# Performance work log

Hardware: AMD Instinct MI355X
Metric: run time of the kernel (lower is better)

## Reference

```python
import jax, jax.numpy as jnp
import numpy as np

D_MODEL = 1024
N_EXPERTS = 16
TOP_K = 2
NUM_TASKS = 8
D_TASK = 64
D_FFN = 32
LN_EPS = 1e-5


def setup_inputs() -> dict:
    key = jax.random.key(0)
    ks = jax.random.split(key, 8)
    B, S = 4, 4096
    s = 0.02
    return dict(
        x=jax.random.normal(ks[0], (B, S, D_MODEL), jnp.float32),
        task_id=jax.random.randint(ks[1], (B,), 0, NUM_TASKS),
        task_emb=jax.random.normal(ks[2], (NUM_TASKS, D_TASK), jnp.float32) * s,
        Wg=jax.random.normal(ks[3], (D_MODEL + D_TASK, N_EXPERTS), jnp.float32) * s,
        bg=jnp.zeros((N_EXPERTS,), jnp.float32),
        W1=jax.random.normal(ks[4], (N_EXPERTS, D_MODEL, D_FFN), jnp.float32) * s,
        b1=jnp.zeros((N_EXPERTS, D_FFN), jnp.float32),
        W2=jax.random.normal(ks[5], (N_EXPERTS, D_FFN, D_MODEL), jnp.float32) * s,
        b2=jnp.zeros((N_EXPERTS, D_MODEL), jnp.float32),
    )


def reference(x, task_id, task_emb, Wg, bg, W1, b1, W2, b2):
    B, S, D = x.shape
    # F.layer_norm(x, x.shape[1:]): normalize jointly over (seq, d_model), no affine
    mu = jnp.mean(x, axis=(1, 2), keepdims=True)
    var = jnp.var(x, axis=(1, 2), keepdims=True)
    x_norm = (x - mu) * jax.lax.rsqrt(var + LN_EPS)

    t_emb = jnp.broadcast_to(task_emb[task_id][:, None, :], (B, S, D_TASK))
    logits = jnp.concatenate([x_norm, t_emb], axis=-1) @ Wg + bg  # [B,S,E]

    topk_vals, topk_idx = jax.lax.top_k(logits, TOP_K)  # [B,S,K]
    topk_probs = jax.nn.softmax(topk_vals, axis=-1)

    # combine weights per token per expert: w[t,e] = sum_k prob * onehot(idx)
    oh = jax.nn.one_hot(topk_idx, N_EXPERTS, dtype=x.dtype)  # [B,S,K,E]
    w = jnp.einsum('bske,bsk->bse', oh, topk_probs).reshape(B * S, N_EXPERTS)

    xf = x.reshape(B * S, D)
    # all-expert FFN (d_ffn=32 -> small intermediate [T,E,32])
    h = jax.nn.silu(jnp.einsum('td,edf->tef', xf, W1) + b1)
    hw = h * w[:, :, None]  # apply combine weight before expanding back to d_model
    out = jnp.einsum('tef,efd->td', hw, W2) + w @ b2
    final = out.reshape(B, S, D)

    # load-balance loss from expert usage counts
    usage = jnp.sum(oh, axis=(0, 1, 2))  # [E]
    usage_mean = usage.mean() + 1e-6
    usage_std = jnp.std(usage, ddof=1)  # torch unbiased std
    lb_loss = (usage_std / usage_mean) ** 2
    return final, lb_loss, topk_idx
```

## Files before the change

kernel.cpp:

```cpp
#include <hip/hip_runtime.h>
#include <math.h>

#define D_MODEL 1024
#define N_EXP   16
#define SEQ     4096
#define NBATCH  4
#define NTOK    (NBATCH*SEQ)
#define DFFN    32
#define DTASK   64

#define WS_SUMS   0
#define WS_RS     64
#define WS_MU     80
#define WS_GB     128
#define WS_CNT    512
#define WS_TOKREC 1024
#define WS_BUCKET (1024 + NTOK*16)

#define OUT_LB  (NTOK*D_MODEL)
#define OUT_IDX (NTOK*D_MODEL + 1)

__device__ __forceinline__ void atomAddF(float* p, float v) {
  unsafeAtomicAdd(p, v);
}

__global__ __launch_bounds__(256) void k_stats(const float* __restrict__ x,
                                               double* __restrict__ sums) {
  int b = blockIdx.y;
  const float4* xb = (const float4*)(x + (size_t)b * SEQ * D_MODEL);
  const int n4 = SEQ * D_MODEL / 4;
  double s = 0.0, ss = 0.0;
  for (int i = blockIdx.x * 256 + threadIdx.x; i < n4; i += gridDim.x * 256) {
    float4 v = xb[i];
    s  += (double)v.x + (double)v.y + (double)v.z + (double)v.w;
    ss += (double)v.x*v.x + (double)v.y*v.y + (double)v.z*v.z + (double)v.w*v.w;
  }
  __shared__ double r0[256], r1[256];
  r0[threadIdx.x] = s; r1[threadIdx.x] = ss;
  __syncthreads();
  for (int off = 128; off > 0; off >>= 1) {
    if (threadIdx.x < off) { r0[threadIdx.x] += r0[threadIdx.x+off]; r1[threadIdx.x] += r1[threadIdx.x+off]; }
    __syncthreads();
  }
  if (threadIdx.x == 0) { atomicAdd(&sums[2*b], r0[0]); atomicAdd(&sums[2*b+1], r1[0]); }
}

__global__ __launch_bounds__(256) void k_prep(const double* __restrict__ sums,
    const int* __restrict__ task_id, const float* __restrict__ task_emb,
    const float* __restrict__ Wg, const float* __restrict__ bg,
    float* __restrict__ wsf) {
  __shared__ float smu[4], srs[4], sSe[16];
  __shared__ float red[16][16];
  int tid = threadIdx.x;
  if (tid < 4) {
    double n = (double)SEQ * (double)D_MODEL;
    double mu = sums[2*tid] / n;
    double var = sums[2*tid+1] / n - mu*mu;
    float rsv = (float)(1.0 / sqrt(var + 1e-5));
    smu[tid] = (float)mu; srs[tid] = rsv;
    wsf[WS_RS/4 + tid] = rsv; wsf[WS_MU/4 + tid] = (float)mu;
  }
  {
    int e = tid & 15, part = tid >> 4;
    float p = 0.f;
    for (int r = part*64; r < part*64 + 64; ++r) p += Wg[r*N_EXP + e];
    red[part][e] = p;
  }
  __syncthreads();
  if (tid < 16) {
    float t = 0.f;
    for (int i = 0; i < 16; ++i) t += red[i][tid];
    sSe[tid] = t;
  }
  __syncthreads();
  if (tid < 64) {
    int b = tid >> 4, e = tid & 15;
    int tk = task_id[b];
    float off = 0.f;
    for (int j = 0; j < DTASK; ++j)
      off += task_emb[tk*DTASK + j] * Wg[(D_MODEL + j)*N_EXP + e];
    wsf[WS_GB/4 + tid] = bg[e] + off - srs[b]*smu[b]*sSe[e];
  }
}

__global__ __launch_bounds__(256) void k_gating(const float* __restrict__ x,
    const float* __restrict__ Wg, const float* __restrict__ wsf,
    float* __restrict__ out, float4* __restrict__ tokrec,
    int* __restrict__ cnt, int* __restrict__ bucket) {
  __shared__ float wgT[N_EXP][D_MODEL + 1];
  __shared__ float lg[4][4][16];
  int tid = threadIdx.x;
  for (int i = tid; i < D_MODEL*N_EXP/4; i += 256) {
    float4 v = ((const float4*)Wg)[i];
    int d = i >> 2, e0 = (i & 3) << 2;
    wgT[e0+0][d] = v.x; wgT[e0+1][d] = v.y; wgT[e0+2][d] = v.z; wgT[e0+3][d] = v.w;
  }
  __syncthreads();
  int wave = tid >> 6, lane = tid & 63;
  int blk0 = blockIdx.x * 64;
  int b = blk0 >> 12;
  float rsb = wsf[WS_RS/4 + b];
  for (int it = 0; it < 4; ++it) {
    int tbase = blk0 + wave*16 + it*4;
    float xr[4][16];
    #pragma unroll
    for (int tt = 0; tt < 4; ++tt) {
      const float* xp = x + (size_t)(tbase + tt)*D_MODEL + lane;
      #pragma unroll
      for (int j = 0; j < 16; ++j) xr[tt][j] = xp[j*64];
    }
    float v[64];
    #pragma unroll
    for (int i = 0; i < 64; ++i) v[i] = 0.f;
    #pragma unroll
    for (int j = 0; j < 16; ++j) {
      int d = lane + 64*j;
      #pragma unroll
      for (int e = 0; e < 16; ++e) {
        float w = wgT[e][d];
        #pragma unroll
        for (int tt = 0; tt < 4; ++tt) v[tt*16 + e] = fmaf(xr[tt][j], w, v[tt*16 + e]);
      }
    }
    #pragma unroll
    for (int m = 32; m >= 1; m >>= 1) {
      #pragma unroll
      for (int j2 = 0; j2 < m; ++j2) {
        float lo = v[j2], hi = v[j2 + m];
        bool up = (lane & m) != 0;
        float mine = up ? hi : lo;
        float theirs = up ? lo : hi;
        v[j2] = mine + __shfl_xor(theirs, m, 64);
      }
    }
    int e = lane & 15, tt = lane >> 4;
    float logit = fmaf(rsb, v[0], wsf[WS_GB/4 + b*16 + e]);
    lg[wave][tt][e] = logit;
    __syncthreads();
    if ((lane & 15) == 0) {
      int token = tbase + tt;
      float v0 = -1e30f, v1 = -1e30f; int i0 = 0, i1 = 0;
      #pragma unroll
      for (int ee = 0; ee < 16; ++ee) {
        float L = lg[wave][tt][ee];
        if (L > v0)      { v1 = v0; i1 = i0; v0 = L; i0 = ee; }
        else if (L > v1) { v1 = L; i1 = ee; }
      }
      float ex = __expf(v1 - v0);
      float p0 = 1.f / (1.f + ex);
      float p1 = ex * p0;
      out[OUT_IDX + token*2 + 0] = (float)i0;
      out[OUT_IDX + token*2 + 1] = (float)i1;
      tokrec[token] = make_float4(__int_as_float(i0), __int_as_float(i1), p0, p1);
      int pos0 = atomicAdd(&cnt[i0], 1);
      bucket[i0*NTOK + pos0] = token;
      int pos1 = atomicAdd(&cnt[16 + i1], 1);
      bucket[16*NTOK + i1*NTOK + pos1] = token;
    }
    __syncthreads();
  }
}

template<int MODE>
__global__ __launch_bounds__(256) void k_ffn(const float* __restrict__ x,
    const float* __restrict__ W1, const float* __restrict__ b1,
    const float* __restrict__ W2, const float* __restrict__ b2,
    const float4* __restrict__ tokrec, const int* __restrict__ cnt,
    const int* __restrict__ bucket, float* __restrict__ out) {
  int e = blockIdx.y;
  int cntE = cnt[MODE*16 + e];
  int r0 = blockIdx.x * 64;
  if (r0 >= cntE) return;
  int R = min(64, cntE - r0);

  __shared__ int   toks[64];
  __shared__ float wself[64], woth[64];
  __shared__ int   eoth[64];
  __shared__ float xT[64][66];
  __shared__ float w1c[64*DFFN];
  __shared__ float hwT[DFFN][72];

  int tid = threadIdx.x;
  if (tid < 64) {
    int idx = (tid < R) ? (r0 + tid) : r0;
    int tok = bucket[MODE*16*NTOK + e*NTOK + idx];
    toks[tid] = tok;
    float4 rec = tokrec[tok];
    if (MODE == 0) { wself[tid] = rec.z; woth[tid] = rec.w; eoth[tid] = __float_as_int(rec.y); }
    else           { wself[tid] = rec.w; }
  }
  __syncthreads();

  float acc[2][4] = {};
  int tg = tid >> 3, fg = tid & 7;
  const float* W1e = W1 + (size_t)e * D_MODEL * DFFN;
  int lr = tid >> 2, lq = tid & 3;

  for (int kc = 0; kc < D_MODEL; kc += 64) {
    const float* xrow = x + (size_t)toks[lr]*D_MODEL + kc + lq*16;
    float4 a0 = *(const float4*)(xrow + 0);
    float4 a1 = *(const float4*)(xrow + 4);
    float4 a2 = *(const float4*)(xrow + 8);
    float4 a3 = *(const float4*)(xrow + 12);
    const float4* w1g = (const float4*)(W1e + kc*DFFN);
    float4 wr0 = w1g[tid*2], wr1 = w1g[tid*2 + 1];
    __syncthreads();
    int kb = lq * 16;
    xT[kb+ 0][lr]=a0.x; xT[kb+ 1][lr]=a0.y; xT[kb+ 2][lr]=a0.z; xT[kb+ 3][lr]=a0.w;
    xT[kb+ 4][lr]=a1.x; xT[kb+ 5][lr]=a1.y; xT[kb+ 6][lr]=a1.z; xT[kb+ 7][lr]=a1.w;
    xT[kb+ 8][lr]=a2.x; xT[kb+ 9][lr]=a2.y; xT[kb+10][lr]=a2.z; xT[kb+11][lr]=a2.w;
    xT[kb+12][lr]=a3.x; xT[kb+13][lr]=a3.y; xT[kb+14][lr]=a3.z; xT[kb+15][lr]=a3.w;
    ((float4*)w1c)[tid*2] = wr0; ((float4*)w1c)[tid*2 + 1] = wr1;
    __syncthreads();
    #pragma unroll
    for (int kk = 0; kk < 64; ++kk) {
      float2 xv = *(const float2*)&xT[kk][2*tg];
      float4 wv = *(const float4*)&w1c[kk*DFFN + 4*fg];
      acc[0][0] = fmaf(xv.x, wv.x, acc[0][0]);
      acc[0][1] = fmaf(xv.x, wv.y, acc[0][1]);
      acc[0][2] = fmaf(xv.x, wv.z, acc[0][2]);
      acc[0][3] = fmaf(xv.x, wv.w, acc[0][3]);
      acc[1][0] = fmaf(xv.y, wv.x, acc[1][0]);
      acc[1][1] = fmaf(xv.y, wv.y, acc[1][1]);
      acc[1][2] = fmaf(xv.y, wv.z, acc[1][2]);
      acc[1][3] = fmaf(xv.y, wv.w, acc[1][3]);
    }
  }
  #pragma unroll
  for (int tt = 0; tt < 2; ++tt) {
    int row = 2*tg + tt;
    float wsv = wself[row];
    #pragma unroll
    for (int ff = 0; ff < 4; ++ff) {
      int f = 4*fg + ff;
      float hp = acc[tt][ff] + b1[e*DFFN + f];
      float sg = 1.f / (1.f + __expf(-hp));
      hwT[f][row] = hp * sg * wsv;
    }
  }
  __syncthreads();

  int d0 = tid << 2;
  const float* W2e = W2 + (size_t)e * DFFN * D_MODEL;
  const float* b2e = b2 + (size_t)e * D_MODEL;
  for (int g = 0; g < 8; ++g) {
    float4 acc2[8];
    #pragma unroll
    for (int t = 0; t < 8; ++t) {
      if (MODE == 0) {
        int row = 8*g + t;
        float4 bs = *(const float4*)(b2e + d0);
        float4 bo = *(const float4*)(b2 + (size_t)eoth[row]*D_MODEL + d0);
        float w0 = wself[row], w1 = woth[row];
        acc2[t] = make_float4(w0*bs.x + w1*bo.x, w0*bs.y + w1*bo.y,
                              w0*bs.z + w1*bo.z, w0*bs.w + w1*bo.w);
      } else {
        acc2[t] = make_float4(0.f, 0.f, 0.f, 0.f);
      }
    }
    #pragma unroll 8
    for (int f = 0; f < DFFN; ++f) {
      float4 w2v = *(const float4*)(W2e + (size_t)f*D_MODEL + d0);
      const float* hp = &hwT[f][8*g];
      #pragma unroll
      for (int t = 0; t < 8; ++t) {
        float hv = hp[t];
        acc2[t].x = fmaf(hv, w2v.x, acc2[t].x);
        acc2[t].y = fmaf(hv, w2v.y, acc2[t].y);
        acc2[t].z = fmaf(hv, w2v.z, acc2[t].z);
        acc2[t].w = fmaf(hv, w2v.w, acc2[t].w);
      }
    }
    #pragma unroll
    for (int t = 0; t < 8; ++t) {
      int row = 8*g + t;
      if (row < R) {
        float* op = out + (size_t)toks[row]*D_MODEL + d0;
        if (MODE == 0) {
          *(float4*)op = acc2[t];
        } else {
          atomAddF(op+0, acc2[t].x); atomAddF(op+1, acc2[t].y);
          atomAddF(op+2, acc2[t].z); atomAddF(op+3, acc2[t].w);
        }
      }
    }
  }
}

__global__ void k_lb(const int* __restrict__ cnt, float* __restrict__ out) {
  if (threadIdx.x == 0 && blockIdx.x == 0) {
    float u[16]; float s = 0.f;
    for (int e = 0; e < 16; ++e) { u[e] = (float)(cnt[e] + cnt[16 + e]); s += u[e]; }
    float mean = s / 16.f;
    float var = 0.f;
    for (int e = 0; e < 16; ++e) { float d = u[e] - mean; var += d*d; }
    var /= 15.f;
    float m = mean + 1e-6f;
    out[OUT_LB] = var / (m*m);
  }
}

extern "C" void kernel_launch(void* const* d_in, const int* in_sizes, int n_in,
                              void* d_out, int out_size, void* d_ws, size_t ws_size,
                              hipStream_t stream) {
  const float* x        = (const float*)d_in[0];
  const int*   task_id  = (const int*)  d_in[1];
  const float* task_emb = (const float*)d_in[2];
  const float* Wg       = (const float*)d_in[3];
  const float* bg       = (const float*)d_in[4];
  const float* W1       = (const float*)d_in[5];
  const float* b1       = (const float*)d_in[6];
  const float* W2       = (const float*)d_in[7];
  const float* b2       = (const float*)d_in[8];
  float* out = (float*)d_out;
  char* ws = (char*)d_ws;
  double* sums   = (double*)(ws + WS_SUMS);
  float*  wsf    = (float*) ws;
  float4* tokrec = (float4*)(ws + WS_TOKREC);
  int*    cnt    = (int*)   (ws + WS_CNT);
  int*    bucket = (int*)   (ws + WS_BUCKET);

  hipMemsetAsync(ws, 0, 1024, stream);
  k_stats<<<dim3(128, 4), 256, 0, stream>>>(x, sums);
  k_prep<<<1, 256, 0, stream>>>(sums, task_id, task_emb, Wg, bg, wsf);
  k_gating<<<NTOK/64, 256, 0, stream>>>(x, Wg, wsf, out, tokrec, cnt, bucket);
  k_ffn<0><<<dim3(256, 16), 256, 0, stream>>>(x, W1, b1, W2, b2, tokrec, cnt, bucket, out);
  k_ffn<1><<<dim3(256, 16), 256, 0, stream>>>(x, W1, b1, W2, b2, tokrec, cnt, bucket, out);
  k_lb<<<1, 64, 0, stream>>>(cnt, out);
}
```

Baseline: 654.8 us.

## Split expert FFN into separate up-projection and down-projection kernels with prefetching

Replaces the fused per-expert FFN kernel with two stages. k_h computes x·W1 + b1 for every (slot, expert) bucket into a compacted workspace buffer, using offsets from a new prefix-sum kernel and register double-buffered loads of the x and W1 tiles. k_o then applies SiLU and the combine weight, stages W2 chunks in shared memory with register prefetch, and writes or atomically adds the outputs. The aim is better reuse of W2 and overlap of global loads with compute. The cost is an extra round trip through global memory for h, and the grids cap each bucket at 6144 tokens.

```diff
diff --git a/kernel.cpp b/kernel.cpp
--- a/kernel.cpp
+++ b/kernel.cpp
@@ -8,20 +8,31 @@
 #define NTOK    (NBATCH*SEQ)
 #define DFFN    32
 #define DTASK   64
+#define NASSIGN (2*NTOK)
 
 #define WS_SUMS   0
 #define WS_RS     64
 #define WS_MU     80
 #define WS_GB     128
 #define WS_CNT    512
+#define WS_OFF    640
 #define WS_TOKREC 1024
 #define WS_BUCKET (1024 + NTOK*16)
+#define WS_H      (WS_BUCKET + 32*NTOK*4)
 
 #define OUT_LB  (NTOK*D_MODEL)
 #define OUT_IDX (NTOK*D_MODEL + 1)
 
 __device__ __forceinline__ void atomAddF(float* p, float v) {
   unsafeAtomicAdd(p, v);
+}
+__device__ __forceinline__ float4 fma4(float s, float4 w, float4 a) {
+  a.x = fmaf(s, w.x, a.x); a.y = fmaf(s, w.y, a.y);
+  a.z = fmaf(s, w.z, a.z); a.w = fmaf(s, w.w, a.w);
+  return a;
+}
+__device__ __forceinline__ float siluw(float v, float w) {
+  return w * v / (1.f + __expf(-v));
 }
 
 __global__ __launch_bounds__(256) void k_stats(const float* __restrict__ x,
@@ -161,142 +172,227 @@
   }
 }
 
-template<int MODE>
-__global__ __launch_bounds__(256) void k_ffn(const float* __restrict__ x,
-    const float* __restrict__ W1, const float* __restrict__ b1,
-    const float* __restrict__ W2, const float* __restrict__ b2,
-    const float4* __restrict__ tokrec, const int* __restrict__ cnt,
-    const int* __restrict__ bucket, float* __restrict__ out) {
-  int e = blockIdx.y;
-  int cntE = cnt[MODE*16 + e];
-  int r0 = blockIdx.x * 64;
-  if (r0 >= cntE) return;
-  int R = min(64, cntE - r0);
-
-  __shared__ int   toks[64];
-  __shared__ float wself[64], woth[64];
-  __shared__ int   eoth[64];
-  __shared__ float xT[64][66];
-  __shared__ float w1c[64*DFFN];
-  __shared__ float hwT[DFFN][72];
-
-  int tid = threadIdx.x;
-  if (tid < 64) {
-    int idx = (tid < R) ? (r0 + tid) : r0;
-    int tok = bucket[MODE*16*NTOK + e*NTOK + idx];
-    toks[tid] = tok;
-    float4 rec = tokrec[tok];
-    if (MODE == 0) { wself[tid] = rec.z; woth[tid] = rec.w; eoth[tid] = __float_as_int(rec.y); }
-    else           { wself[tid] = rec.w; }
-  }
-  __syncthreads();
-
-  float acc[2][4] = {};
-  int tg = tid >> 3, fg = tid & 7;
-  const float* W1e = W1 + (size_t)e * D_MODEL * DFFN;
-  int lr = tid >> 2, lq = tid & 3;
-
-  for (int kc = 0; kc < D_MODEL; kc += 64) {
-    const float* xrow = x + (size_t)toks[lr]*D_MODEL + kc + lq*16;
-    float4 a0 = *(const float4*)(xrow + 0);
-    float4 a1 = *(const float4*)(xrow + 4);
-    float4 a2 = *(const float4*)(xrow + 8);
-    float4 a3 = *(const float4*)(xrow + 12);
-    const float4* w1g = (const float4*)(W1e + kc*DFFN);
-    float4 wr0 = w1g[tid*2], wr1 = w1g[tid*2 + 1];
-    __syncthreads();
-    int kb = lq * 16;
-    xT[kb+ 0][lr]=a0.x; xT[kb+ 1][lr]=a0.y; xT[kb+ 2][lr]=a0.z; xT[kb+ 3][lr]=a0.w;
-    xT[kb+ 4][lr]=a1.x; xT[kb+ 5][lr]=a1.y; xT[kb+ 6][lr]=a1.z; xT[kb+ 7][lr]=a1.w;
-    xT[kb+ 8][lr]=a2.x; xT[kb+ 9][lr]=a2.y; xT[kb+10][lr]=a2.z; xT[kb+11][lr]=a2.w;
-    xT[kb+12][lr]=a3.x; xT[kb+13][lr]=a3.y; xT[kb+14][lr]=a3.z; xT[kb+15][lr]=a3.w;
-    ((float4*)w1c)[tid*2] = wr0; ((float4*)w1c)[tid*2 + 1] = wr1;
-    __syncthreads();
-    #pragma unroll
-    for (int kk = 0; kk < 64; ++kk) {
-      float2 xv = *(const float2*)&xT[kk][2*tg];
-      float4 wv = *(const float4*)&w1c[kk*DFFN + 4*fg];
-      acc[0][0] = fmaf(xv.x, wv.x, acc[0][0]);
-      acc[0][1] = fmaf(xv.x, wv.y, acc[0][1]);
-      acc[0][2] = fmaf(xv.x, wv.z, acc[0][2]);
-      acc[0][3] = fmaf(xv.x, wv.w, acc[0][3]);
-      acc[1][0] = fmaf(xv.y, wv.x, acc[1][0]);
-      acc[1][1] = fmaf(xv.y, wv.y, acc[1][1]);
-      acc[1][2] = fmaf(xv.y, wv.z, acc[1][2]);
-      acc[1][3] = fmaf(xv.y, wv.w, acc[1][3]);
-    }
-  }
-  #pragma unroll
-  for (int tt = 0; tt < 2; ++tt) {
-    int row = 2*tg + tt;
-    float wsv = wself[row];
-    #pragma unroll
-    for (int ff = 0; ff < 4; ++ff) {
-      int f = 4*fg + ff;
-      float hp = acc[tt][ff] + b1[e*DFFN + f];
-      float sg = 1.f / (1.f + __expf(-hp));
-      hwT[f][row] = hp * sg * wsv;
-    }
-  }
-  __syncthreads();
-
-  int d0 = tid << 2;
-  const float* W2e = W2 + (size_t)e * DFFN * D_MODEL;
-  const float* b2e = b2 + (size_t)e * D_MODEL;
-  for (int g = 0; g < 8; ++g) {
-    float4 acc2[8];
-    #pragma unroll
-    for (int t = 0; t < 8; ++t) {
-      if (MODE == 0) {
-        int row = 8*g + t;
-        float4 bs = *(const float4*)(b2e + d0);
-        float4 bo = *(const float4*)(b2 + (size_t)eoth[row]*D_MODEL + d0);
-        float w0 = wself[row], w1 = woth[row];
-        acc2[t] = make_float4(w0*bs.x + w1*bo.x, w0*bs.y + w1*bo.y,
-                              w0*bs.z + w1*bo.z, w0*bs.w + w1*bo.w);
-      } else {
-        acc2[t] = make_float4(0.f, 0.f, 0.f, 0.f);
-      }
-    }
-    #pragma unroll 8
-    for (int f = 0; f < DFFN; ++f) {
-      float4 w2v = *(const float4*)(W2e + (size_t)f*D_MODEL + d0);
-      const float* hp = &hwT[f][8*g];
-      #pragma unroll
-      for (int t = 0; t < 8; ++t) {
-        float hv = hp[t];
-        acc2[t].x = fmaf(hv, w2v.x, acc2[t].x);
-        acc2[t].y = fmaf(hv, w2v.y, acc2[t].y);
-        acc2[t].z = fmaf(hv, w2v.z, acc2[t].z);
-        acc2[t].w = fmaf(hv, w2v.w, acc2[t].w);
-      }
-    }
-    #pragma unroll
-    for (int t = 0; t < 8; ++t) {
-      int row = 8*g + t;
-      if (row < R) {
-        float* op = out + (size_t)toks[row]*D_MODEL + d0;
-        if (MODE == 0) {
-          *(float4*)op = acc2[t];
-        } else {
-          atomAddF(op+0, acc2[t].x); atomAddF(op+1, acc2[t].y);
-          atomAddF(op+2, acc2[t].z); atomAddF(op+3, acc2[t].w);
-        }
-      }
-    }
-  }
-}
-
-__global__ void k_lb(const int* __restrict__ cnt, float* __restrict__ out) {
+__global__ void k_off_lb(const int* __restrict__ cnt, int* __restrict__ off,
+                         float* __restrict__ out) {
   if (threadIdx.x == 0 && blockIdx.x == 0) {
-    float u[16]; float s = 0.f;
-    for (int e = 0; e < 16; ++e) { u[e] = (float)(cnt[e] + cnt[16 + e]); s += u[e]; }
-    float mean = s / 16.f;
-    float var = 0.f;
+    int s = 0;
+    for (int ke = 0; ke < 32; ++ke) { off[ke] = s; s += cnt[ke]; }
+    float u[16], tot = 0.f;
+    for (int e = 0; e < 16; ++e) { u[e] = (float)(cnt[e] + cnt[16+e]); tot += u[e]; }
+    float mean = tot / 16.f, var = 0.f;
     for (int e = 0; e < 16; ++e) { float d = u[e] - mean; var += d*d; }
     var /= 15.f;
     float m = mean + 1e-6f;
     out[OUT_LB] = var / (m*m);
+  }
+}
+
+#define HT 64
+#define BK 64
+__global__ __launch_bounds__(256) void k_h(const float* __restrict__ x,
+    const float* __restrict__ W1, const float* __restrict__ b1,
+    const int* __restrict__ cnt, const int* __restrict__ off,
+    const int* __restrict__ bucket, float* __restrict__ h) {
+  int ke = blockIdx.y, e = ke & 15;
+  int cntE = cnt[ke];
+  int r0 = blockIdx.x * HT;
+  if (r0 >= cntE) return;
+  int R = min(HT, cntE - r0);
+  __shared__ int toks[HT];
+  __shared__ float xs[HT][BK + 4];
+  __shared__ float w1s[BK * DFFN];
+  int tid = threadIdx.x;
+  if (tid < HT) toks[tid] = bucket[ke * NTOK + ((tid < R) ? (r0 + tid) : r0)];
+  __syncthreads();
+  int lr = tid >> 2, lq = tid & 3;
+  int a2 = tid >> 3, fg = tid & 7;
+  const float* W1e = W1 + (size_t)e * D_MODEL * DFFN;
+  const float* xrow = x + (size_t)toks[lr] * D_MODEL + lq * 16;
+  float4 xa[4], wa[2];
+  xa[0] = *(const float4*)(xrow + 0);
+  xa[1] = *(const float4*)(xrow + 4);
+  xa[2] = *(const float4*)(xrow + 8);
+  xa[3] = *(const float4*)(xrow + 12);
+  {
+    const float4* wg = (const float4*)W1e;
+    wa[0] = wg[tid]; wa[1] = wg[tid + 256];
+  }
+  float4 acc0 = make_float4(0,0,0,0), acc1 = make_float4(0,0,0,0);
+  #pragma unroll 1
+  for (int c = 0; c < D_MODEL / BK; ++c) {
+    if (c) __syncthreads();
+    *(float4*)&xs[lr][lq*16 + 0]  = xa[0];
+    *(float4*)&xs[lr][lq*16 + 4]  = xa[1];
+    *(float4*)&xs[lr][lq*16 + 8]  = xa[2];
+    *(float4*)&xs[lr][lq*16 + 12] = xa[3];
+    ((float4*)w1s)[tid]       = wa[0];
+    ((float4*)w1s)[tid + 256] = wa[1];
+    __syncthreads();
+    if (c + 1 < D_MODEL / BK) {
+      const float* xn = xrow + (c + 1) * BK;
+      xa[0] = *(const float4*)(xn + 0);
+      xa[1] = *(const float4*)(xn + 4);
+      xa[2] = *(const float4*)(xn + 8);
+      xa[3] = *(const float4*)(xn + 12);
+      const float4* wg = (const float4*)(W1e + (c + 1) * BK * DFFN);
+      wa[0] = wg[tid]; wa[1] = wg[tid + 256];
+    }
+    #pragma unroll
+    for (int kk = 0; kk < BK; kk += 4) {
+      float4 xv0 = *(const float4*)&xs[2*a2][kk];
+      float4 xv1 = *(const float4*)&xs[2*a2+1][kk];
+      const float* wb = &w1s[kk * DFFN + 4 * fg];
+      float4 w0  = *(const float4*)(wb);
+      float4 w1r = *(const float4*)(wb + DFFN);
+      float4 w2r = *(const float4*)(wb + 2*DFFN);
+      float4 w3r = *(const float4*)(wb + 3*DFFN);
+      acc0 = fma4(xv0.x, w0,  acc0); acc1 = fma4(xv1.x, w0,  acc1);
+      acc0 = fma4(xv0.y, w1r, acc0); acc1 = fma4(xv1.y, w1r, acc1);
+      acc0 = fma4(xv0.z, w2r, acc0); acc1 = fma4(xv1.z, w2r, acc1);
+      acc0 = fma4(xv0.w, w3r, acc0); acc1 = fma4(xv1.w, w3r, acc1);
+    }
+  }
+  float4 b1v = *(const float4*)(b1 + e * DFFN + 4 * fg);
+  acc0.x += b1v.x; acc0.y += b1v.y; acc0.z += b1v.z; acc0.w += b1v.w;
+  acc1.x += b1v.x; acc1.y += b1v.y; acc1.z += b1v.z; acc1.w += b1v.w;
+  int base = off[ke] + r0;
+  if (2*a2 < R)     *(float4*)&h[(size_t)(base + 2*a2)     * DFFN + 4*fg] = acc0;
+  if (2*a2 + 1 < R) *(float4*)&h[(size_t)(base + 2*a2 + 1) * DFFN + 4*fg] = acc1;
+}
+
+#define OT 32
+#define DCH 256
+template<int MODE>
+__global__ __launch_bounds__(256) void k_o(const float* __restrict__ h,
+    const float* __restrict__ W2, const float* __restrict__ b2,
+    const float4* __restrict__ tokrec, const int* __restrict__ cnt,
+    const int* __restrict__ off, const int* __restrict__ bucket,
+    float* __restrict__ out) {
+  int e = blockIdx.y, ke = MODE * 16 + e;
+  int cntE = cnt[ke];
+  int r0 = blockIdx.x * OT;
+  if (r0 >= cntE) return;
+  int R = min(OT, cntE - r0);
+  __shared__ float w2s[DFFN][DCH];
+  __shared__ int toks[OT], eo[OT];
+  __shared__ float wsl[OT], wot[OT];
+  int tid = threadIdx.x;
+  if (tid < OT) {
+    int tok = bucket[ke * NTOK + ((tid < R) ? (r0 + tid) : r0)];
+    toks[tid] = tok;
+    float4 rec = tokrec[tok];
+    if (MODE == 0) { wsl[tid] = rec.z; wot[tid] = rec.w; eo[tid] = __float_as_int(rec.y); }
+    else           { wsl[tid] = rec.w; }
+  }
+  __syncthreads();
+  int t2 = tid >> 4, dg = tid & 15;
+  int ta = 2 * t2, tb = ta + 1;
+  int tokA = toks[ta], tokB = toks[tb];
+  float wA = wsl[ta], wB = wsl[tb];
+  float hwA[DFFN], hwB[DFFN];
+  {
+    int base = off[ke] + r0;
+    const float4* hA = (const float4*)(h + (size_t)(base + ta) * DFFN);
+    const float4* hB = (const float4*)(h + (size_t)(base + tb) * DFFN);
+    #pragma unroll
+    for (int q = 0; q < 8; ++q) {
+      float4 a = hA[q], b = hB[q];
+      hwA[4*q+0] = siluw(a.x, wA); hwA[4*q+1] = siluw(a.y, wA);
+      hwA[4*q+2] = siluw(a.z, wA); hwA[4*q+3] = siluw(a.w, wA);
+      hwB[4*q+0] = siluw(b.x, wB); hwB[4*q+1] = siluw(b.y, wB);
+      hwB[4*q+2] = siluw(b.z, wB); hwB[4*q+3] = siluw(b.w, wB);
+    }
+  }
+  const float* W2e = W2 + (size_t)e * DFFN * D_MODEL;
+  float4 st[8];
+  #pragma unroll
+  for (int i = 0; i < 8; ++i) {
+    int idx = tid + i * 256;
+    st[i] = *(const float4*)(W2e + (size_t)(idx >> 6) * D_MODEL + ((idx & 63) << 2));
+  }
+  #pragma unroll 1
+  for (int dc = 0; dc < D_MODEL / DCH; ++dc) {
+    if (dc) __syncthreads();
+    #pragma unroll
+    for (int i = 0; i < 8; ++i) {
+      int idx = tid + i * 256;
+      *(float4*)&w2s[idx >> 6][(idx & 63) << 2] = st[i];
+    }
+    __syncthreads();
+    if (dc + 1 < D_MODEL / DCH) {
+      #pragma unroll
+      for (int i = 0; i < 8; ++i) {
+        int idx = tid + i * 256;
+        st[i] = *(const float4*)(W2e + (size_t)(idx >> 6) * D_MODEL
+                                 + (dc + 1) * DCH + ((idx & 63) << 2));
+      }
+    }
+    int d0 = dg * 4;
+    float4 aA[4], aB[4];
+    if (MODE == 0) {
+      const float* bsE = b2 + (size_t)e * D_MODEL + dc * DCH + d0;
+      const float* boA = b2 + (size_t)eo[ta] * D_MODEL + dc * DCH + d0;
+      const float* boB = b2 + (size_t)eo[tb] * D_MODEL + dc * DCH + d0;
+      float woA = wot[ta], woB = wot[tb];
+      #pragma unroll
+      for (int j = 0; j < 4; ++j) {
+        float4 bs = *(const float4*)(bsE + 64 * j);
+        float4 bA = *(const float4*)(boA + 64 * j);
+        float4 bB = *(const float4*)(boB + 64 * j);
+        aA[j] = make_float4(wA*bs.x + woA*bA.x, wA*bs.y + woA*bA.y,
+                            wA*bs.z + woA*bA.z, wA*bs.w + woA*bA.w);
+        aB[j] = make_float4(wB*bs.x + woB*bB.x, wB*bs.y + woB*bB.y,
+                            wB*bs.z + woB*bB.z, wB*bs.w + woB*bB.w);
+      }
+    } else {
+      #pragma unroll
+      for (int j = 0; j < 4; ++j) {
+        aA[j] = make_float4(0.f, 0.f, 0.f, 0.f);
+        aB[j] = make_float4(0.f, 0.f, 0.f, 0.f);
+      }
+    }
+    #pragma unroll
+    for (int f = 0; f < DFFN; ++f) {
+      const float* wb = &w2s[f][d0];
+      float4 w0  = *(const float4*)(wb);
+      float4 w1r = *(const float4*)(wb + 64);
+      float4 w2r = *(const float4*)(wb + 128);
+      float4 w3r = *(const float4*)(wb + 192);
+      float ha = hwA[f], hb = hwB[f];
+      aA[0] = fma4(ha, w0,  aA[0]); aA[1] = fma4(ha, w1r, aA[1]);
+      aA[2] = fma4(ha, w2r, aA[2]); aA[3] = fma4(ha, w3r, aA[3]);
+      aB[0] = fma4(hb, w0,  aB[0]); aB[1] = fma4(hb, w1r, aB[1]);
+      aB[2] = fma4(hb, w2r, aB[2]); aB[3] = fma4(hb, w3r, aB[3]);
+    }
+    float* oA = out + (size_t)tokA * D_MODEL + dc * DCH + d0;
+    float* oB = out + (size_t)tokB * D_MODEL + dc * DCH + d0;
+    if (MODE == 0) {
+      if (ta < R) {
+        #pragma unroll
+        for (int j = 0; j < 4; ++j) *(float4*)(oA + 64 * j) = aA[j];
+      }
+      if (tb < R) {
+        #pragma unroll
+        for (int j = 0; j < 4; ++j) *(float4*)(oB + 64 * j) = aB[j];
+      }
+    } else {
+      if (ta < R) {
+        #pragma unroll
+        for (int j = 0; j < 4; ++j) {
+          float* p = oA + 64 * j;
+          atomAddF(p+0, aA[j].x); atomAddF(p+1, aA[j].y);
+          atomAddF(p+2, aA[j].z); atomAddF(p+3, aA[j].w);
+        }
+      }
+      if (tb < R) {
+        #pragma unroll
+        for (int j = 0; j < 4; ++j) {
+          float* p = oB + 64 * j;
+          atomAddF(p+0, aB[j].x); atomAddF(p+1, aB[j].y);
+          atomAddF(p+2, aB[j].z); atomAddF(p+3, aB[j].w);
+        }
+      }
+    }
   }
 }
 
@@ -318,13 +414,16 @@
   float*  wsf    = (float*) ws;
   float4* tokrec = (float4*)(ws + WS_TOKREC);
   int*    cnt    = (int*)   (ws + WS_CNT);
+  int*    off    = (int*)   (ws + WS_OFF);
   int*    bucket = (int*)   (ws + WS_BUCKET);
+  float*  h      = (float*) (ws + WS_H);
 
   hipMemsetAsync(ws, 0, 1024, stream);
   k_stats<<<dim3(128, 4), 256, 0, stream>>>(x, sums);
   k_prep<<<1, 256, 0, stream>>>(sums, task_id, task_emb, Wg, bg, wsf);
   k_gating<<<NTOK/64, 256, 0, stream>>>(x, Wg, wsf, out, tokrec, cnt, bucket);
-  k_ffn<0><<<dim3(256, 16), 256, 0, stream>>>(x, W1, b1, W2, b2, tokrec, cnt, bucket, out);
-  k_ffn<1><<<dim3(256, 16), 256, 0, stream>>>(x, W1, b1, W2, b2, tokrec, cnt, bucket, out);
-  k_lb<<<1, 64, 0, stream>>>(cnt, out);
-}
+  k_off_lb<<<1, 64, 0, stream>>>(cnt, off, out);
+  k_h<<<dim3(96, 32), 256, 0, stream>>>(x, W1, b1, cnt, off, bucket, h);
+  k_o<0><<<dim3(192, 16), 256, 0, stream>>>(h, W2, b2, tokrec, cnt, off, bucket, out);
+  k_o<1><<<dim3(192, 16), 256, 0, stream>>>(h, W2, b2, tokrec, cnt, off, bucket, out);
+}
```

Measured after the change: 1.403 ms. 2.14x slower.
